# Performance work log

Hardware: AMD Instinct MI355X
Metric: run time of the kernel (lower is better)

Reference implementation:

```python
import jax, jax.numpy as jnp
import numpy as np

NUM_CLASSES = 2
BG_PID = 5532
NUM_ROIS = 128          # cfg.TRAIN.BATCH_SIZE
NUM_FG_MAX = 32         # round(cfg.TRAIN.FG_FRACTION * BATCH_SIZE), FG_FRACTION = 0.25
FG_THRESH = 0.5
BG_THRESH_HI = 0.5
BG_THRESH_LO = 0.1
MEANS = jnp.array([0.0, 0.0, 0.0, 0.0], dtype=jnp.float32)
STDS = jnp.array([0.1, 0.1, 0.2, 0.2], dtype=jnp.float32)
INSIDE_W = jnp.array([1.0, 1.0, 1.0, 1.0], dtype=jnp.float32)


def _make_boxes(key, n, img_w=1000.0, img_h=600.0):
    k1, k2, k3, k4 = jax.random.split(key, 4)
    x1 = jax.random.uniform(k1, (n,)) * (img_w - 330.0)
    y1 = jax.random.uniform(k2, (n,)) * (img_h - 350.0)
    w = 20.0 + jax.random.uniform(k3, (n,)) * 300.0
    h = 40.0 + jax.random.uniform(k4, (n,)) * 300.0
    return jnp.stack([x1, y1, x1 + w, y1 + h], axis=1).astype(jnp.float32)


def setup_inputs() -> dict:
    key = jax.random.key(0)
    kr, kg, kp = jax.random.split(key, 3)
    R, G = 131072, 256
    rois = _make_boxes(kr, R)
    all_rois = jnp.concatenate([jnp.zeros((R, 1), jnp.float32), rois], axis=1)  # [R,5]
    gtb = _make_boxes(kg, G)
    labels = jnp.ones((G, 1), jnp.float32)  # person class = 1
    pids = jax.random.randint(kp, (G, 1), 0, BG_PID).astype(jnp.float32)
    gt_boxes = jnp.concatenate([gtb, labels, pids], axis=1)  # [G,6]
    return {"all_rois": all_rois, "gt_boxes": gt_boxes}


def bbox_overlaps(a, b):
    iw = jnp.minimum(a[:, None, 2], b[None, :, 2]) - jnp.maximum(a[:, None, 0], b[None, :, 0]) + 1.0
    ih = jnp.minimum(a[:, None, 3], b[None, :, 3]) - jnp.maximum(a[:, None, 1], b[None, :, 1]) + 1.0
    iw = jnp.maximum(iw, 0.0)
    ih = jnp.maximum(ih, 0.0)
    area_a = (a[:, 2] - a[:, 0] + 1.0) * (a[:, 3] - a[:, 1] + 1.0)
    area_b = (b[:, 2] - b[:, 0] + 1.0) * (b[:, 3] - b[:, 1] + 1.0)
    inter = iw * ih
    return inter / (area_a[:, None] + area_b[None, :] - inter)


def bbox_transform(ex, gt):
    ew = ex[:, 2] - ex[:, 0] + 1.0
    eh = ex[:, 3] - ex[:, 1] + 1.0
    ecx = ex[:, 0] + 0.5 * ew
    ecy = ex[:, 1] + 0.5 * eh
    gw = gt[:, 2] - gt[:, 0] + 1.0
    gh = gt[:, 3] - gt[:, 1] + 1.0
    gcx = gt[:, 0] + 0.5 * gw
    gcy = gt[:, 1] + 0.5 * gh
    return jnp.stack([(gcx - ecx) / ew, (gcy - ecy) / eh,
                      jnp.log(gw / ew), jnp.log(gh / eh)], axis=1)


def _forward(all_rois, gt_boxes):
    G = gt_boxes.shape[0]
    gt_rois = jnp.concatenate([jnp.zeros((G, 1), all_rois.dtype), gt_boxes[:, :4]], axis=1)
    rois_all = jnp.concatenate([all_rois, gt_rois], axis=0)  # [R+G,5]
    N = rois_all.shape[0]
    overlaps = bbox_overlaps(rois_all[:, 1:5], gt_boxes[:, :4])  # [R+G, G]
    argmax_ov = jnp.argmax(overlaps, axis=1)
    max_ov = jnp.max(overlaps, axis=1)
    labels_all = gt_boxes[argmax_ov, 4]
    pids_all = gt_boxes[argmax_ov, 5]
    fg_mask = max_ov >= FG_THRESH
    bg_mask = (max_ov < BG_THRESH_HI) & (max_ov >= BG_THRESH_LO)
    num_fg = jnp.minimum(jnp.int32(NUM_FG_MAX), fg_mask.sum().astype(jnp.int32))
    num_bg = jnp.minimum(jnp.int32(NUM_ROIS) - num_fg, bg_mask.sum().astype(jnp.int32))
    # deterministic 'take first k' selection (DEBUG path of the original),
    # expressed as a fixed-shape scatter: rank within fg/bg -> output slot
    fg_rank = (jnp.cumsum(fg_mask) - 1).astype(jnp.int32)
    bg_rank = (jnp.cumsum(bg_mask) - 1).astype(jnp.int32)
    idx = jnp.arange(N, dtype=jnp.int32)
    pos_fg = jnp.where(fg_mask & (fg_rank < num_fg), fg_rank, jnp.int32(NUM_ROIS))
    pos_bg = jnp.where(bg_mask & (bg_rank < num_bg), num_fg + bg_rank, jnp.int32(NUM_ROIS))
    keep = jnp.zeros((NUM_ROIS,), jnp.int32)
    keep = keep.at[pos_fg].set(idx, mode="drop")
    keep = keep.at[pos_bg].set(idx, mode="drop")
    slot_is_fg = jnp.arange(NUM_ROIS) < num_fg
    rois = rois_all[keep]                                   # [128,5]
    labels = jnp.where(slot_is_fg, labels_all[keep], 0.0)
    pids = jnp.where(slot_is_fg, pids_all[keep], jnp.float32(BG_PID))
    tgt = bbox_transform(rois[:, 1:5], gt_boxes[argmax_ov[keep], :4])
    tgt = (tgt - MEANS) / STDS
    cls = jnp.round(labels).astype(jnp.int32)
    onehot = jax.nn.one_hot(cls, NUM_CLASSES, dtype=tgt.dtype) * (labels > 0).astype(tgt.dtype)[:, None]
    bbox_targets = (onehot[:, :, None] * tgt[:, None, :]).reshape(NUM_ROIS, 4 * NUM_CLASSES)
    bbox_inside = (onehot[:, :, None] * INSIDE_W[None, None, :]).reshape(NUM_ROIS, 4 * NUM_CLASSES)
    bbox_outside = (onehot[:, :, None] * jnp.ones((4,), tgt.dtype)).reshape(NUM_ROIS, 4 * NUM_CLASSES)
    return rois, labels, pids, bbox_targets, bbox_inside, bbox_outside


def reference(all_rois, gt_boxes):
    rois, labels, pids, bt, bi, bo = _forward(all_rois, gt_boxes)
    return rois, labels.astype(jnp.int32), pids.astype(jnp.int32), bt, bi, bo
```

## Files before the change

### kernel.cpp

```cpp
#include <hip/hip_runtime.h>
#include <stdint.h>

#define OUT_ROIS 128
#define FG_MAX 32
#define BG_PID_F 5532.0f
#define MAXCH 2304


__global__ __launch_bounds__(256, 4) void ptl_classify(
    const float* __restrict__ all_rois, const float* __restrict__ gt,
    int R, int G, int N,
    uint8_t* __restrict__ code, int* __restrict__ blkF, int* __restrict__ blkB)
{
#pragma clang fp contract(off)
    __shared__ float4 g4[256];
    __shared__ float  gA[256];
    __shared__ uint8_t flg[4][128];
    const int t = threadIdx.x;
    const int w = t >> 6, lane = t & 63;

    if (t < G) {
        const float* p = gt + (size_t)t * 6;
        const float a = p[0], b = p[1], c = p[2], d = p[3];
        g4[t] = make_float4(a, b, c, d);
        gA[t] = ((c - a) + 1.0f) * ((d - b) + 1.0f);
    }
    __syncthreads();

    const int base = blockIdx.x * 128;
    float x1a, y1a, x2a, y2a, x1b, y1b, x2b, y2b;
    {
        const int i0 = base + lane;
        if (i0 < N) {
            if (i0 < R) { const float* p = all_rois + (size_t)i0 * 5; x1a=p[1]; y1a=p[2]; x2a=p[3]; y2a=p[4]; }
            else        { const float* p = gt + (size_t)(i0 - R) * 6; x1a=p[0]; y1a=p[1]; x2a=p[2]; y2a=p[3]; }
        } else { x1a=0.0f; y1a=0.0f; x2a=-2.0f; y2a=-2.0f; }
        const int i1 = base + 64 + lane;
        if (i1 < N) {
            if (i1 < R) { const float* p = all_rois + (size_t)i1 * 5; x1b=p[1]; y1b=p[2]; x2b=p[3]; y2b=p[4]; }
            else        { const float* p = gt + (size_t)(i1 - R) * 6; x1b=p[0]; y1b=p[1]; x2b=p[2]; y2b=p[3]; }
        } else { x1b=0.0f; y1b=0.0f; x2b=-2.0f; y2b=-2.0f; }
    }
    const float Aa = ((x2a - x1a) + 1.0f) * ((y2a - y1a) + 1.0f);
    const float Ab = ((x2b - x1b) + 1.0f) * ((y2b - y1b) + 1.0f);

    float aF0 = -1e38f, aB0 = -1e38f, aF1 = -1e38f, aB1 = -1e38f;

#define IOU2(QQ, GAv)                                                   \
    do {                                                                \
        const float4 q_ = (QQ); const float ga_ = (GAv);                \
        {   float iw = (fminf(x2a, q_.z) - fmaxf(x1a, q_.x)) + 1.0f;    \
            float ih = (fminf(y2a, q_.w) - fmaxf(y1a, q_.y)) + 1.0f;    \
            iw = fmaxf(iw, 0.0f); ih = fmaxf(ih, 0.0f);                 \
            const float I = iw * ih;                                    \
            const float D = (Aa + ga_) - I;                             \
            const float h  = fmaf(-0.5f, D, I);                         \
            const float gF = fmaf(0x1p-26f, D, h);                      \
            const float h2 = fmaf(-0.1f, D, I);                         \
            const float gB = fmaf(0x1p-28f, D, h2);                     \
            aF0 = fmaxf(aF0, gF); aB0 = fmaxf(aB0, gB); }               \
        {   float iw = (fminf(x2b, q_.z) - fmaxf(x1b, q_.x)) + 1.0f;    \
            float ih = (fminf(y2b, q_.w) - fmaxf(y1b, q_.y)) + 1.0f;    \
            iw = fmaxf(iw, 0.0f); ih = fmaxf(ih, 0.0f);                 \
            const float I = iw * ih;                                    \
            const float D = (Ab + ga_) - I;                             \
            const float h  = fmaf(-0.5f, D, I);                         \
            const float gF = fmaf(0x1p-26f, D, h);                      \
            const float h2 = fmaf(-0.1f, D, I);                         \
            const float gB = fmaf(0x1p-28f, D, h2);                     \
            aF1 = fmaxf(aF1, gF); aB1 = fmaxf(aB1, gB); }               \
    } while (0)

    if (G == 256) {
        const int jbeg = w * 64;
        float4 qb0[8], qb1[8];
        float  ga0[8], ga1[8];
#pragma unroll
        for (int u = 0; u < 8; ++u) { qb0[u] = g4[jbeg + u]; ga0[u] = gA[jbeg + u]; }
#pragma unroll
        for (int grp = 0; grp < 8; ++grp) {
            if ((grp & 1) == 0) {
                if (grp + 1 < 8) {
#pragma unroll
                    for (int u = 0; u < 8; ++u) {
                        qb1[u] = g4[jbeg + (grp + 1) * 8 + u];
                        ga1[u] = gA[jbeg + (grp + 1) * 8 + u];
                    }
                }
#pragma unroll
                for (int u = 0; u < 8; ++u) IOU2(qb0[u], ga0[u]);
            } else {
                if (grp + 1 < 8) {
#pragma unroll
                    for (int u = 0; u < 8; ++u) {
                        qb0[u] = g4[jbeg + (grp + 1) * 8 + u];
                        ga0[u] = gA[jbeg + (grp + 1) * 8 + u];
                    }
                }
#pragma unroll
                for (int u = 0; u < 8; ++u) IOU2(qb1[u], ga1[u]);
            }
        }
    } else {
        const int jbeg = (G * w) >> 2, jend = (G * (w + 1)) >> 2;
        for (int j = jbeg; j < jend; ++j) IOU2(g4[j], gA[j]);
    }
#undef IOU2

    flg[w][lane]      = (uint8_t)((aF0 >= 0.0f ? 1u : 0u) | (aB0 > 0.0f ? 2u : 0u));
    flg[w][64 + lane] = (uint8_t)((aF1 >= 0.0f ? 1u : 0u) | (aB1 > 0.0f ? 2u : 0u));
    __syncthreads();

    if (t < 128) {
        const uint32_t u = (uint32_t)flg[0][t] | flg[1][t] | flg[2][t] | flg[3][t];
        const int cls = (u & 1u) ? 1 : ((u & 2u) ? 2 : 0);
        const int i2 = base + t;
        if (i2 < N) code[i2] = (uint8_t)cls;
        unsigned long long mF = __ballot(cls == 1);
        unsigned long long mB = __ballot(cls == 2);
        if ((t & 63) == 0) {
            blkF[blockIdx.x * 2 + (t >> 6)] = __popcll(mF);
            blkB[blockIdx.x * 2 + (t >> 6)] = __popcll(mB);
        }
    }
}

__global__ __launch_bounds__(256) void ptl_select_emit(
    const float* __restrict__ all_rois, const float* __restrict__ gt,
    const uint8_t* __restrict__ code,
    const int* __restrict__ blkF, const int* __restrict__ blkB,
    int R, int G, int N, int nch,
    float* __restrict__ out)
{
#pragma clang fp contract(off)
    __shared__ int sF[MAXCH], sB[MAXCH];
    __shared__ int EF[MAXCH], EB[MAXCH];
    __shared__ int tsF[256], tsB[256];
    __shared__ int keep[OUT_ROIS];
    __shared__ int sam[OUT_ROIS];
    __shared__ int nwork;
    __shared__ unsigned short work[MAXCH];
    const int t = threadIdx.x;

    for (int c = t; c < nch; c += 256) { sF[c] = blkF[c]; sB[c] = blkB[c]; }
    for (int c = nch + t; c < MAXCH; c += 256) { sF[c] = 0; sB[c] = 0; }
    if (t < OUT_ROIS) { keep[t] = 0; sam[t] = 0; }
    if (t == 0) nwork = 0;
    __syncthreads();

    const int c0 = t * (MAXCH / 256);
    int baseF = 0, baseB = 0;
#pragma unroll
    for (int k = 0; k < MAXCH / 256; ++k) { baseF += sF[c0 + k]; baseB += sB[c0 + k]; }
    tsF[t] = baseF; tsB[t] = baseB;
    __syncthreads();
    for (int d = 1; d < 256; d <<= 1) {
        int vF = (t >= d) ? tsF[t - d] : 0;
        int vB = (t >= d) ? tsB[t - d] : 0;
        __syncthreads();
        tsF[t] += vF; tsB[t] += vB;
        __syncthreads();
    }
    const int tf = tsF[255], tb = tsB[255];
    const int num_fg = tf < FG_MAX ? tf : FG_MAX;
    const int rem = OUT_ROIS - num_fg;
    const int num_bg = tb < rem ? tb : rem;

    int rF = tsF[t] - baseF, rB = tsB[t] - baseB;
#pragma unroll
    for (int k = 0; k < MAXCH / 256; ++k) {
        const int c = c0 + k;
        const int cf = sF[c], cb = sB[c];
        EF[c] = rF; EB[c] = rB;
        const bool need = ((cf > 0 && rF < num_fg) || (cb > 0 && rB < num_bg)) && (c < nch);
        if (need) { int p = atomicAdd(&nwork, 1); work[p] = (unsigned short)c; }
        rF += cf; rB += cb;
    }
    __syncthreads();

    const int w = t >> 6, lane = t & 63;
    const unsigned long long lowmask = (1ull << lane) - 1ull;
    const int nw = nwork;
    for (int idx = w; idx < nw; idx += 4) {
        const int c = work[idx];
        const int i = c * 64 + lane;
        const int cd = (i < N) ? (int)code[i] : 0;
        unsigned long long mF = __ballot(cd == 1);
        unsigned long long mB = __ballot(cd == 2);
        const int pF = EF[c] + __popcll(mF & lowmask);
        const int pB = EB[c] + __popcll(mB & lowmask);
        if (cd == 1 && pF < num_fg) keep[pF] = i;
        if (cd == 2 && pB < num_bg) keep[num_fg + pB] = i;
    }
    __syncthreads();

    for (int s = w; s < num_fg; s += 4) {
        const int k = keep[s];
        float x1, y1, x2, y2;
        if (k < R) { const float* p = all_rois + (size_t)k * 5; x1=p[1]; y1=p[2]; x2=p[3]; y2=p[4]; }
        else       { const float* p = gt + (size_t)(k - R) * 6; x1=p[0]; y1=p[1]; x2=p[2]; y2=p[3]; }
        const float A = ((x2 - x1) + 1.0f) * ((y2 - y1) + 1.0f);
        float mv = -1.0f; int mj = 0;
        for (int jj = 0; jj < 4; ++jj) {
            const int j = jj * 64 + lane;
            float iou = -1.0f;
            if (j < G) {
                const float* p = gt + (size_t)j * 6;
                const float a = p[0], b = p[1], c2 = p[2], d2 = p[3];
                const float ga = ((c2 - a) + 1.0f) * ((d2 - b) + 1.0f);
                float iw = (fminf(x2, c2) - fmaxf(x1, a)) + 1.0f;
                float ih = (fminf(y2, d2) - fmaxf(y1, b)) + 1.0f;
                iw = fmaxf(iw, 0.0f); ih = fmaxf(ih, 0.0f);
                const float inter = iw * ih;
                iou = inter / ((A + ga) - inter);
            }
            if (iou > mv) { mv = iou; mj = j; }
        }
#pragma unroll
        for (int m = 1; m < 64; m <<= 1) {
            const float ov = __shfl_xor(mv, m);
            const int oj = __shfl_xor(mj, m);
            if (ov > mv || (ov == mv && oj < mj)) { mv = ov; mj = oj; }
        }
        if (lane == 0) sam[s] = mj;
    }
    __syncthreads();

    if (t < OUT_ROIS) {
        const int s = t;
        const int k = keep[s];
        const bool isfg = s < num_fg;
        float x1, y1, x2, y2;
        if (k < R) { const float* p = all_rois + (size_t)k * 5; x1=p[1]; y1=p[2]; x2=p[3]; y2=p[4]; }
        else       { const float* p = gt + (size_t)(k - R) * 6; x1=p[0]; y1=p[1]; x2=p[2]; y2=p[3]; }
        const int amax = sam[s];
        const float* g = gt + (size_t)amax * 6;
        const float gx1v = g[0], gy1v = g[1], gx2v = g[2], gy2v = g[3];
        const float label = isfg ? g[4] : 0.0f;
        const float pid = isfg ? g[5] : BG_PID_F;

        float* ro = out + (size_t)s * 5;
        ro[0] = 0.0f; ro[1] = x1; ro[2] = y1; ro[3] = x2; ro[4] = y2;
        out[640 + s] = (float)(int)label;
        out[768 + s] = (float)(int)pid;

        const float ew = (x2 - x1) + 1.0f, eh = (y2 - y1) + 1.0f;
        const float ecx = x1 + 0.5f * ew, ecy = y1 + 0.5f * eh;
        const float gw = (gx2v - gx1v) + 1.0f, gh = (gy2v - gy1v) + 1.0f;
        const float gcx = gx1v + 0.5f * gw, gcy = gy1v + 0.5f * gh;
        float tv[4];
        tv[0] = ((gcx - ecx) / ew) / 0.1f;
        tv[1] = ((gcy - ecy) / eh) / 0.1f;
        tv[2] = logf(gw / ew) / 0.2f;
        tv[3] = logf(gh / eh) / 0.2f;

        const int cls = (int)roundf(label);
        const float on = (label > 0.0f) ? 1.0f : 0.0f;

        float* bt = out + 896  + (size_t)s * 8;
        float* bi = out + 1920 + (size_t)s * 8;
        float* bo = out + 2944 + (size_t)s * 8;
#pragma unroll
        for (int cc = 0; cc < 2; ++cc) {
            const float sel = (cc == cls) ? on : 0.0f;
#pragma unroll
            for (int j = 0; j < 4; ++j) {
                bt[cc * 4 + j] = sel * tv[j];
                bi[cc * 4 + j] = sel;
                bo[cc * 4 + j] = sel;
            }
        }
    }
}

extern "C" void kernel_launch(void* const* d_in, const int* in_sizes, int n_in,
                              void* d_out, int out_size, void* d_ws, size_t ws_size,
                              hipStream_t stream) {
    const float* all_rois = (const float*)d_in[0];
    const float* gt       = (const float*)d_in[1];
    const int R = in_sizes[0] / 5;
    const int G = in_sizes[1] / 6;
    const int N = R + G;
    const int nblk = (N + 127) / 128;
    const int nch = (N + 63) / 64;

    uint8_t* code = (uint8_t*)d_ws;
    size_t codeBytes = ((size_t)N + 255) & ~(size_t)255;
    int* blkF = (int*)((char*)d_ws + codeBytes);
    int* blkB = blkF + 2 * nblk;
    float* out = (float*)d_out;

    ptl_classify<<<nblk, 256, 0, stream>>>(all_rois, gt, R, G, N, code, blkF, blkB);
    ptl_select_emit<<<1, 256, 0, stream>>>(all_rois, gt, code, blkF, blkB, R, G, N, nch, out);
}
```

Before: 37.84 us.

## Fuse classify and select kernels via last-block-done tail with shared union

Merges the classification kernel and the single-block selection/emit kernel into one launch. An atomic done counter elects the last finishing block to run the prefix scan, selection and emit, reusing a shared-memory union so occupancy is unchanged. Per-chunk prefix offsets are packed into the work list, saturated to 255, in place of separate EF/EB arrays. The fg argmax now uses 8 lanes per ROI instead of a full wave. It adds a memset launch and threadfence ordering, and the saturation relies on the fg and bg counts staying small.

```diff
diff --git a/kernel.cpp b/kernel.cpp
--- a/kernel.cpp
+++ b/kernel.cpp
@@ -7,23 +7,38 @@
 #define MAXCH 2304
 
 
-__global__ __launch_bounds__(256, 4) void ptl_classify(
+union SharedU {
+    struct {
+        float4  g4[256];
+        float   gA[256];
+        uint8_t flg[4][128];
+    } c;
+    struct {
+        int      sF[MAXCH], sB[MAXCH];
+        int      tsF[256], tsB[256];
+        int      keep[OUT_ROIS], sam[OUT_ROIS];
+        uint32_t work[MAXCH];
+        int      nwork;
+    } s;
+};
+
+__global__ __launch_bounds__(256, 4) void ptl_fused(
     const float* __restrict__ all_rois, const float* __restrict__ gt,
-    int R, int G, int N,
-    uint8_t* __restrict__ code, int* __restrict__ blkF, int* __restrict__ blkB)
+    int R, int G, int N, int nch,
+    uint8_t* __restrict__ code, int* __restrict__ blkF, int* __restrict__ blkB,
+    int* __restrict__ done, float* __restrict__ out)
 {
 #pragma clang fp contract(off)
-    __shared__ float4 g4[256];
-    __shared__ float  gA[256];
-    __shared__ uint8_t flg[4][128];
+    __shared__ SharedU u;
+    __shared__ int isTail;
     const int t = threadIdx.x;
     const int w = t >> 6, lane = t & 63;
 
     if (t < G) {
         const float* p = gt + (size_t)t * 6;
         const float a = p[0], b = p[1], c = p[2], d = p[3];
-        g4[t] = make_float4(a, b, c, d);
-        gA[t] = ((c - a) + 1.0f) * ((d - b) + 1.0f);
+        u.c.g4[t] = make_float4(a, b, c, d);
+        u.c.gA[t] = ((c - a) + 1.0f) * ((d - b) + 1.0f);
     }
     __syncthreads();
 
@@ -76,46 +91,47 @@
         float4 qb0[8], qb1[8];
         float  ga0[8], ga1[8];
 #pragma unroll
-        for (int u = 0; u < 8; ++u) { qb0[u] = g4[jbeg + u]; ga0[u] = gA[jbeg + u]; }
+        for (int uu = 0; uu < 8; ++uu) { qb0[uu] = u.c.g4[jbeg + uu]; ga0[uu] = u.c.gA[jbeg + uu]; }
 #pragma unroll
         for (int grp = 0; grp < 8; ++grp) {
             if ((grp & 1) == 0) {
                 if (grp + 1 < 8) {
 #pragma unroll
-                    for (int u = 0; u < 8; ++u) {
-                        qb1[u] = g4[jbeg + (grp + 1) * 8 + u];
-                        ga1[u] = gA[jbeg + (grp + 1) * 8 + u];
+                    for (int uu = 0; uu < 8; ++uu) {
+                        qb1[uu] = u.c.g4[jbeg + (grp + 1) * 8 + uu];
+                        ga1[uu] = u.c.gA[jbeg + (grp + 1) * 8 + uu];
                     }
                 }
 #pragma unroll
-                for (int u = 0; u < 8; ++u) IOU2(qb0[u], ga0[u]);
+                for (int uu = 0; uu < 8; ++uu) IOU2(qb0[uu], ga0[uu]);
             } else {
                 if (grp + 1 < 8) {
 #pragma unroll
-                    for (int u = 0; u < 8; ++u) {
-                        qb0[u] = g4[jbeg + (grp + 1) * 8 + u];
-                        ga0[u] = gA[jbeg + (grp + 1) * 8 + u];
+                    for (int uu = 0; uu < 8; ++uu) {
+                        qb0[uu] = u.c.g4[jbeg + (grp + 1) * 8 + uu];
+                        ga0[uu] = u.c.gA[jbeg + (grp + 1) * 8 + uu];
                     }
                 }
 #pragma unroll
-                for (int u = 0; u < 8; ++u) IOU2(qb1[u], ga1[u]);
+                for (int uu = 0; uu < 8; ++uu) IOU2(qb1[uu], ga1[uu]);
             }
         }
     } else {
         const int jbeg = (G * w) >> 2, jend = (G * (w + 1)) >> 2;
-        for (int j = jbeg; j < jend; ++j) IOU2(g4[j], gA[j]);
+        for (int j = jbeg; j < jend; ++j) IOU2(u.c.g4[j], u.c.gA[j]);
     }
 #undef IOU2
 
-    flg[w][lane]      = (uint8_t)((aF0 >= 0.0f ? 1u : 0u) | (aB0 > 0.0f ? 2u : 0u));
-    flg[w][64 + lane] = (uint8_t)((aF1 >= 0.0f ? 1u : 0u) | (aB1 > 0.0f ? 2u : 0u));
+    u.c.flg[w][lane]      = (uint8_t)((aF0 >= 0.0f ? 1u : 0u) | (aB0 > 0.0f ? 2u : 0u));
+    u.c.flg[w][64 + lane] = (uint8_t)((aF1 >= 0.0f ? 1u : 0u) | (aB1 > 0.0f ? 2u : 0u));
     __syncthreads();
 
     if (t < 128) {
-        const uint32_t u = (uint32_t)flg[0][t] | flg[1][t] | flg[2][t] | flg[3][t];
-        const int cls = (u & 1u) ? 1 : ((u & 2u) ? 2 : 0);
+        const uint32_t uf = (uint32_t)u.c.flg[0][t] | u.c.flg[1][t] | u.c.flg[2][t] | u.c.flg[3][t];
         const int i2 = base + t;
-        if (i2 < N) code[i2] = (uint8_t)cls;
+        int cls = (uf & 1u) ? 1 : ((uf & 2u) ? 2 : 0);
+        if (i2 >= N) cls = 0;
+        else code[i2] = (uint8_t)cls;
         unsigned long long mF = __ballot(cls == 1);
         unsigned long long mB = __ballot(cls == 2);
         if ((t & 63) == 0) {
@@ -123,88 +139,83 @@
             blkB[blockIdx.x * 2 + (t >> 6)] = __popcll(mB);
         }
     }
-}
-
-__global__ __launch_bounds__(256) void ptl_select_emit(
-    const float* __restrict__ all_rois, const float* __restrict__ gt,
-    const uint8_t* __restrict__ code,
-    const int* __restrict__ blkF, const int* __restrict__ blkB,
-    int R, int G, int N, int nch,
-    float* __restrict__ out)
-{
-#pragma clang fp contract(off)
-    __shared__ int sF[MAXCH], sB[MAXCH];
-    __shared__ int EF[MAXCH], EB[MAXCH];
-    __shared__ int tsF[256], tsB[256];
-    __shared__ int keep[OUT_ROIS];
-    __shared__ int sam[OUT_ROIS];
-    __shared__ int nwork;
-    __shared__ unsigned short work[MAXCH];
-    const int t = threadIdx.x;
-
-    for (int c = t; c < nch; c += 256) { sF[c] = blkF[c]; sB[c] = blkB[c]; }
-    for (int c = nch + t; c < MAXCH; c += 256) { sF[c] = 0; sB[c] = 0; }
-    if (t < OUT_ROIS) { keep[t] = 0; sam[t] = 0; }
-    if (t == 0) nwork = 0;
+    __syncthreads();
+
+    if (t == 0) {
+        __threadfence();
+        const int old = atomicAdd(done, 1);
+        isTail = (old == (int)gridDim.x - 1) ? 1 : 0;
+    }
+    __syncthreads();
+    if (!isTail) return;
+    __threadfence();
+
+    for (int c = t; c < nch; c += 256) { u.s.sF[c] = blkF[c]; u.s.sB[c] = blkB[c]; }
+    for (int c = nch + t; c < MAXCH; c += 256) { u.s.sF[c] = 0; u.s.sB[c] = 0; }
+    if (t < OUT_ROIS) { u.s.keep[t] = 0; u.s.sam[t] = 0; }
+    if (t == 0) u.s.nwork = 0;
     __syncthreads();
 
     const int c0 = t * (MAXCH / 256);
     int baseF = 0, baseB = 0;
 #pragma unroll
-    for (int k = 0; k < MAXCH / 256; ++k) { baseF += sF[c0 + k]; baseB += sB[c0 + k]; }
-    tsF[t] = baseF; tsB[t] = baseB;
+    for (int k = 0; k < MAXCH / 256; ++k) { baseF += u.s.sF[c0 + k]; baseB += u.s.sB[c0 + k]; }
+    u.s.tsF[t] = baseF; u.s.tsB[t] = baseB;
     __syncthreads();
     for (int d = 1; d < 256; d <<= 1) {
-        int vF = (t >= d) ? tsF[t - d] : 0;
-        int vB = (t >= d) ? tsB[t - d] : 0;
+        int vF = (t >= d) ? u.s.tsF[t - d] : 0;
+        int vB = (t >= d) ? u.s.tsB[t - d] : 0;
         __syncthreads();
-        tsF[t] += vF; tsB[t] += vB;
+        u.s.tsF[t] += vF; u.s.tsB[t] += vB;
         __syncthreads();
     }
-    const int tf = tsF[255], tb = tsB[255];
+    const int tf = u.s.tsF[255], tb = u.s.tsB[255];
     const int num_fg = tf < FG_MAX ? tf : FG_MAX;
     const int rem = OUT_ROIS - num_fg;
     const int num_bg = tb < rem ? tb : rem;
 
-    int rF = tsF[t] - baseF, rB = tsB[t] - baseB;
+    int rF = u.s.tsF[t] - baseF, rB = u.s.tsB[t] - baseB;
 #pragma unroll
     for (int k = 0; k < MAXCH / 256; ++k) {
         const int c = c0 + k;
-        const int cf = sF[c], cb = sB[c];
-        EF[c] = rF; EB[c] = rB;
+        const int cf = u.s.sF[c], cb = u.s.sB[c];
         const bool need = ((cf > 0 && rF < num_fg) || (cb > 0 && rB < num_bg)) && (c < nch);
-        if (need) { int p = atomicAdd(&nwork, 1); work[p] = (unsigned short)c; }
+        if (need) {
+            const uint32_t efc = (uint32_t)(rF < 255 ? rF : 255);
+            const uint32_t ebc = (uint32_t)(rB < 255 ? rB : 255);
+            const int p = atomicAdd(&u.s.nwork, 1);
+            u.s.work[p] = ((uint32_t)c << 16) | (efc << 8) | ebc;
+        }
         rF += cf; rB += cb;
     }
     __syncthreads();
 
-    const int w = t >> 6, lane = t & 63;
     const unsigned long long lowmask = (1ull << lane) - 1ull;
-    const int nw = nwork;
+    const int nw = u.s.nwork;
     for (int idx = w; idx < nw; idx += 4) {
-        const int c = work[idx];
+        const uint32_t e = u.s.work[idx];
+        const int c = (int)(e >> 16);
         const int i = c * 64 + lane;
         const int cd = (i < N) ? (int)code[i] : 0;
         unsigned long long mF = __ballot(cd == 1);
         unsigned long long mB = __ballot(cd == 2);
-        const int pF = EF[c] + __popcll(mF & lowmask);
-        const int pB = EB[c] + __popcll(mB & lowmask);
-        if (cd == 1 && pF < num_fg) keep[pF] = i;
-        if (cd == 2 && pB < num_bg) keep[num_fg + pB] = i;
-    }
-    __syncthreads();
-
-    for (int s = w; s < num_fg; s += 4) {
-        const int k = keep[s];
-        float x1, y1, x2, y2;
-        if (k < R) { const float* p = all_rois + (size_t)k * 5; x1=p[1]; y1=p[2]; x2=p[3]; y2=p[4]; }
-        else       { const float* p = gt + (size_t)(k - R) * 6; x1=p[0]; y1=p[1]; x2=p[2]; y2=p[3]; }
-        const float A = ((x2 - x1) + 1.0f) * ((y2 - y1) + 1.0f);
-        float mv = -1.0f; int mj = 0;
-        for (int jj = 0; jj < 4; ++jj) {
-            const int j = jj * 64 + lane;
-            float iou = -1.0f;
-            if (j < G) {
+        const int pF = (int)((e >> 8) & 0xFF) + __popcll(mF & lowmask);
+        const int pB = (int)(e & 0xFF) + __popcll(mB & lowmask);
+        if (cd == 1 && pF < num_fg) u.s.keep[pF] = i;
+        if (cd == 2 && pB < num_bg) u.s.keep[num_fg + pB] = i;
+    }
+    __syncthreads();
+
+    {
+        const int grp = t >> 3, l8 = t & 7;
+        if (grp < num_fg) {
+            const int k = u.s.keep[grp];
+            float x1, y1, x2, y2;
+            if (k < R) { const float* p = all_rois + (size_t)k * 5; x1=p[1]; y1=p[2]; x2=p[3]; y2=p[4]; }
+            else       { const float* p = gt + (size_t)(k - R) * 6; x1=p[0]; y1=p[1]; x2=p[2]; y2=p[3]; }
+            const float A = ((x2 - x1) + 1.0f) * ((y2 - y1) + 1.0f);
+            float mv = -1.0f; int mj = 0;
+            for (int j = l8; j < G; j += 8) {
                 const float* p = gt + (size_t)j * 6;
                 const float a = p[0], b = p[1], c2 = p[2], d2 = p[3];
                 const float ga = ((c2 - a) + 1.0f) * ((d2 - b) + 1.0f);
@@ -212,28 +223,28 @@
                 float ih = (fminf(y2, d2) - fmaxf(y1, b)) + 1.0f;
                 iw = fmaxf(iw, 0.0f); ih = fmaxf(ih, 0.0f);
                 const float inter = iw * ih;
-                iou = inter / ((A + ga) - inter);
+                const float iou = inter / ((A + ga) - inter);
+                if (iou > mv) { mv = iou; mj = j; }
             }
-            if (iou > mv) { mv = iou; mj = j; }
-        }
-#pragma unroll
-        for (int m = 1; m < 64; m <<= 1) {
-            const float ov = __shfl_xor(mv, m);
-            const int oj = __shfl_xor(mj, m);
-            if (ov > mv || (ov == mv && oj < mj)) { mv = ov; mj = oj; }
-        }
-        if (lane == 0) sam[s] = mj;
+#pragma unroll
+            for (int m = 1; m < 8; m <<= 1) {
+                const float ov = __shfl_xor(mv, m);
+                const int oj = __shfl_xor(mj, m);
+                if (ov > mv || (ov == mv && oj < mj)) { mv = ov; mj = oj; }
+            }
+            if (l8 == 0) u.s.sam[grp] = mj;
+        }
     }
     __syncthreads();
 
     if (t < OUT_ROIS) {
         const int s = t;
-        const int k = keep[s];
+        const int k = u.s.keep[s];
         const bool isfg = s < num_fg;
         float x1, y1, x2, y2;
         if (k < R) { const float* p = all_rois + (size_t)k * 5; x1=p[1]; y1=p[2]; x2=p[3]; y2=p[4]; }
         else       { const float* p = gt + (size_t)(k - R) * 6; x1=p[0]; y1=p[1]; x2=p[2]; y2=p[3]; }
-        const int amax = sam[s];
+        const int amax = u.s.sam[s];
         const float* g = gt + (size_t)amax * 6;
         const float gx1v = g[0], gy1v = g[1], gx2v = g[2], gy2v = g[3];
         const float label = isfg ? g[4] : 0.0f;
@@ -284,12 +295,14 @@
     const int nblk = (N + 127) / 128;
     const int nch = (N + 63) / 64;
 
-    uint8_t* code = (uint8_t*)d_ws;
+    int* done = (int*)d_ws;
+    uint8_t* code = (uint8_t*)d_ws + 256;
     size_t codeBytes = ((size_t)N + 255) & ~(size_t)255;
-    int* blkF = (int*)((char*)d_ws + codeBytes);
+    int* blkF = (int*)((char*)d_ws + 256 + codeBytes);
     int* blkB = blkF + 2 * nblk;
     float* out = (float*)d_out;
 
-    ptl_classify<<<nblk, 256, 0, stream>>>(all_rois, gt, R, G, N, code, blkF, blkB);
-    ptl_select_emit<<<1, 256, 0, stream>>>(all_rois, gt, code, blkF, blkB, R, G, N, nch, out);
+    hipMemsetAsync(done, 0, sizeof(int), stream);
+    ptl_fused<<<nblk, 256, 0, stream>>>(all_rois, gt, R, G, N, nch,
+                                        code, blkF, blkB, done, out);
 }
```

Measured after the change: 48.58 us. 28.4% more time.
